# Kernel tuning notes

Measured on AMD Instinct MI355X. Metric: run time of the kernel, lower is better.

## Reference

```python
import jax, jax.numpy as jnp
import numpy as np

B, S, H, W, C = 2, 21, 256, 256, 256
Q, NEG = 256, 256
TEMP = 0.5
STRONG_T = 1.0
EPS = 1e-8


def setup_inputs():
    key = jax.random.key(0)
    k1, k2, k3 = jax.random.split(key, 3)
    rep = jax.random.normal(k1, (B, C, H, W), jnp.float32)
    label = jax.random.randint(k2, (B, 1, H, W), 0, S)
    mask = jnp.ones((B, 1, H, W), jnp.float32)
    prob = jax.random.uniform(k3, (B, S, H, W), jnp.float32)
    return {"rep": rep, "label": label, "mask": mask, "prob": prob}


def _cos(a, b, axis=-1):
    # torch.cosine_similarity: dot / (max(|a|,eps) * max(|b|,eps))
    an = jnp.maximum(jnp.linalg.norm(a, axis=axis), EPS)
    bn = jnp.maximum(jnp.linalg.norm(b, axis=axis), EPS)
    return jnp.sum(a * b, axis=axis) / (an * bn)


def _reco_loss(rep, label, mask, prob):
    Sg = prob.shape[1]
    Cf = rep.shape[1]
    lab = label.reshape(-1).astype(jnp.int32)          # [N]
    ignore = lab > Sg - 1
    lab = jnp.where(ignore, 0, lab)
    m = jnp.where(ignore, 0.0, mask.reshape(-1))
    valid = m > 0                                      # [N]
    feats = jnp.transpose(rep, (0, 2, 3, 1)).reshape(-1, Cf)   # [N,C]
    pflat = jnp.transpose(prob, (0, 2, 3, 1)).reshape(-1, Sg)  # [N,S]
    p_lab = jnp.take_along_axis(pflat, lab[:, None], axis=1)[:, 0]
    hard = valid & (p_lab < STRONG_T)

    seg_id = jnp.where(valid, lab, Sg)  # invalid pixels -> overflow bucket Sg
    counts = jax.ops.segment_sum(valid.astype(jnp.int32), seg_id, num_segments=Sg + 1)[:Sg]
    hard_counts = jax.ops.segment_sum(hard.astype(jnp.int32), seg_id, num_segments=Sg + 1)[:Sg]
    proto = jax.ops.segment_sum(feats * valid[:, None].astype(feats.dtype), seg_id,
                                num_segments=Sg + 1)[:Sg]
    proto = proto / jnp.maximum(counts, 1)[:, None].astype(feats.dtype)  # [S,C]

    # stable sort pixels by (segment, hard-first): emulates the per-segment
    # boolean-mask gathers / concatenation order of the torch code
    order = jnp.argsort(seg_id * 2 + (~hard).astype(jnp.int32))
    feats_sorted = feats[order]                                 # [N,C]
    off = jnp.concatenate([jnp.zeros((1,), counts.dtype), jnp.cumsum(counts)[:-1]])

    seg_ids = jnp.arange(Sg)
    keys = jax.random.split(jax.random.key(1), Sg)

    def body(acc, xs):
        i, ki = xs
        ka, kc, kn = jax.random.split(ki, 3)
        # anchors: num_queries random hard pixels of segment i
        hidx = off[i] + jax.random.randint(ka, (Q,), 0, jnp.maximum(hard_counts[i], 1))
        anchor = feats_sorted[hidx]                             # [Q,C]
        # negative class distribution over other segments (rolled order)
        roll = (i + 1 + jnp.arange(Sg - 1)) % Sg
        proto_logits = _cos(proto[i][None, :], proto[roll]) / TEMP  # [S-1]
        samp = jax.random.categorical(kc, proto_logits, shape=(Q, NEG))
        neg_seg = roll[samp]                                    # [Q,NEG]
        # uniform pixel within each sampled segment's block
        u = jax.random.uniform(kn, (Q, NEG))
        nidx = off[neg_seg] + jnp.floor(u * jnp.maximum(counts[neg_seg], 1)).astype(counts.dtype)
        neg_feat = feats_sorted[nidx]                           # [Q,NEG,C]
        all_feat = jnp.concatenate(
            [jnp.broadcast_to(proto[i], (Q, 1, Cf)), neg_feat], axis=1)
        all_feat = jax.lax.stop_gradient(all_feat)              # torch.no_grad block
        seg_logits = _cos(anchor[:, None, :], all_feat) / TEMP  # [Q,1+NEG]
        # cross-entropy with target 0, mean over queries
        ce = jnp.mean(jax.nn.logsumexp(seg_logits, axis=1) - seg_logits[:, 0])
        acc = acc + jnp.where(hard_counts[i] > 0, ce, 0.0)
        return acc, None

    total, _ = jax.lax.scan(body, jnp.float32(0.0), (seg_ids, keys))
    valid_seg = jnp.sum(counts > 0)
    loss = total / jnp.maximum(valid_seg, 1).astype(jnp.float32)
    return jnp.where(valid_seg > 1, loss, jnp.float32(0.0))


def reference(rep, label, mask, prob):
    loss_weight = 1.0
    return loss_weight * _reco_loss(rep, label, mask, prob)
```

## Files before the change

### kernel.cpp

```cpp
#include <hip/hip_runtime.h>
#include <stdint.h>

#define NPIX  131072
#define HW    65536
#define CCH   256
#define NSEG  21
#define NROLL 20
#define QQ    256
#define NNEG  256

typedef float f32x2 __attribute__((ext_vector_type(2)));
typedef __fp16 half2t __attribute__((ext_vector_type(2)));

__device__ __forceinline__ uint64_t rng64(uint32_t i, uint32_t q, uint32_t j) {
  uint64_t x = ((uint64_t)((i << 8) | q) << 32) | (uint64_t)(j * 0x9E3779B1u);
  x ^= 0xD1B54A32D192ED03ULL;
  x += 0x9E3779B97F4A7C15ULL;
  x = (x ^ (x >> 30)) * 0xBF58476D1CE4E5B9ULL;
  x = (x ^ (x >> 27)) * 0x94D049BB133111EBULL;
  return x ^ (x >> 31);
}

__device__ __forceinline__ float fdot2h(half2t a, half2t b, float c) {
  return __builtin_amdgcn_fdot2(a, b, c, false);
}

__device__ __forceinline__ void dec16(uint4 w, half2t* nx) {
  uint32_t dw[4] = { w.x, w.y, w.z, w.w };
#pragma unroll
  for (int d = 0; d < 4; ++d) {
    f32x2 lo = __builtin_amdgcn_cvt_pk_f32_fp8((int)dw[d], false);
    f32x2 hi = __builtin_amdgcn_cvt_pk_f32_fp8((int)dw[d], true);
    nx[d * 2 + 0] = __builtin_amdgcn_cvt_pkrtz(lo.x, lo.y);
    nx[d * 2 + 1] = __builtin_amdgcn_cvt_pkrtz(hi.x, hi.y);
  }
}

__global__ __launch_bounds__(256) void reco_zero(float4* __restrict__ zr, int n4) {
  int idx = blockIdx.x * 256 + threadIdx.x;
  if (idx < n4) zr[idx] = make_float4(0.f, 0.f, 0.f, 0.f);
}

__global__ __launch_bounds__(256) void reco_flags(
    const int* __restrict__ label, const float* __restrict__ mask,
    const float* __restrict__ prob, int* __restrict__ labh,
    int* __restrict__ counts, int* __restrict__ hardc) {
  int row = blockIdx.x;
  int b = row >> 8;
  int h = row & 255;
  int t = threadIdx.x;
  int n = row * 256 + t;

  int lab = label[n];
  bool ignore = lab > NSEG - 1;
  if (ignore) lab = 0;
  float mval = ignore ? 0.f : mask[n];
  bool valid = mval > 0.f;
  float p_lab = prob[(((size_t)b * NSEG + lab) * 256 + h) * 256 + t];
  bool hard = valid && (p_lab < 1.0f);
  labh[n] = lab | (hard ? 32 : 0) | (valid ? 64 : 0);

  __shared__ int cpart[NSEG], hpart[NSEG];
  if (t < NSEG) { cpart[t] = 0; hpart[t] = 0; }
  __syncthreads();
  if (valid) { atomicAdd(&cpart[lab], 1); if (hard) atomicAdd(&hpart[lab], 1); }
  __syncthreads();
  if (t < NSEG) {
    if (cpart[t]) atomicAdd(&counts[t], cpart[t]);
    if (hpart[t]) atomicAdd(&hardc[t], hpart[t]);
  }
}

__global__ void reco_k2t(const int* __restrict__ counts, const int* __restrict__ hardc,
                         int* __restrict__ offs, int* __restrict__ cur_h, int* __restrict__ cur_e) {
  if (threadIdx.x == 0 && blockIdx.x == 0) {
    int o = 0;
    for (int s = 0; s < NSEG; ++s) {
      offs[s] = o;
      cur_h[s] = o;
      cur_e[s] = o + hardc[s];
      o += counts[s];
    }
    offs[NSEG] = o;
  }
}

__global__ __launch_bounds__(256) void reco_k3(const int* __restrict__ labh,
                        int* __restrict__ cur_h, int* __restrict__ cur_e, int* __restrict__ list) {
  int t = threadIdx.x;
  int n = blockIdx.x * 256 + t;
  __shared__ int lcnt[2 * NSEG];
  __shared__ int lbase[2 * NSEG];
  if (t < 2 * NSEG) lcnt[t] = 0;
  __syncthreads();
  int v = labh[n];
  int lab = v & 31;
  bool hard = (v & 32) != 0;
  bool valid = (v & 64) != 0;
  int bucket = lab + (hard ? 0 : NSEG);
  int rank = 0;
  if (valid) rank = atomicAdd(&lcnt[bucket], 1);
  __syncthreads();
  if (t < 2 * NSEG) {
    int c = lcnt[t];
    lbase[t] = c ? atomicAdd((t < NSEG) ? &cur_h[t] : &cur_e[t - NSEG], c) : 0;
  }
  __syncthreads();
  if (valid) list[lbase[bucket] + rank] = n;
}

__global__ __launch_bounds__(256) void reco_k5f(const float* __restrict__ rep,
                        uint8_t* __restrict__ f8, float* __restrict__ norms) {
  int bid = blockIdx.x;
  int wtile = bid & 3;
  int row = bid >> 2;
  int b = row >> 8, h = row & 255;
  int w0 = wtile * 64;
  int t = threadIdx.x;

  __shared__ float tile[64][257];
  __shared__ float partial[4][64];
  __shared__ float inv[64];

  const float* repb = rep + (size_t)b * CCH * HW + (size_t)h * 256 + w0;
  int w4 = t & 15;
  int cbase = t >> 4;
#pragma unroll
  for (int it = 0; it < 16; ++it) {
    int c = it * 16 + cbase;
    float4 v = *(const float4*)&repb[(size_t)c * HW + w4 * 4];
    tile[w4 * 4 + 0][c] = v.x;
    tile[w4 * 4 + 1][c] = v.y;
    tile[w4 * 4 + 2][c] = v.z;
    tile[w4 * 4 + 3][c] = v.w;
  }
  __syncthreads();

  {
    int w = t & 63, qtr = t >> 6;
    float acc = 0.f;
#pragma unroll 8
    for (int cc = 0; cc < 64; ++cc) {
      float v = tile[w][qtr * 64 + cc];
      acc += v * v;
    }
    partial[qtr][w] = acc;
  }
  __syncthreads();
  if (t < 64) {
    float s = partial[0][t] + partial[1][t] + partial[2][t] + partial[3][t];
    float nm = fmaxf(sqrtf(s), 1e-8f);
    inv[t] = 1.0f / nm;
    norms[row * 256 + w0 + t] = nm;
  }
  __syncthreads();

  int pix = t & 7, chunk = t >> 3;
#pragma unroll
  for (int it = 0; it < 8; ++it) {
    int p = it * 8 + pix;
    float iv = inv[p];
    float v[8];
#pragma unroll
    for (int k = 0; k < 8; ++k) v[k] = tile[p][chunk * 8 + k] * iv;
    uint32_t lo = 0, hi = 0;
    lo = (uint32_t)__builtin_amdgcn_cvt_pk_fp8_f32(v[0], v[1], (int)lo, false);
    lo = (uint32_t)__builtin_amdgcn_cvt_pk_fp8_f32(v[2], v[3], (int)lo, true);
    hi = (uint32_t)__builtin_amdgcn_cvt_pk_fp8_f32(v[4], v[5], (int)hi, false);
    hi = (uint32_t)__builtin_amdgcn_cvt_pk_fp8_f32(v[6], v[7], (int)hi, true);
    size_t n = (size_t)(row * 256 + w0 + p);
    uint2 o; o.x = lo; o.y = hi;
    *(uint2*)&f8[n * CCH + chunk * 8] = o;
  }
}

__global__ __launch_bounds__(256) void reco_proto8(
    const uint8_t* __restrict__ f8, const float* __restrict__ norms,
    const int* __restrict__ list, const int* __restrict__ labh,
    const int* __restrict__ offs, float* __restrict__ proto) {
  int t = threadIdx.x;
  int base = blockIdx.x * 256;
  int total = offs[NSEG];

  __shared__ uint8_t rows[64][256];
  __shared__ float nrm[64];
  __shared__ int segs[256];
  __shared__ int pixs[256];
  __shared__ float red[64][17];

  {
    int pos = base + t;
    int p = (pos < total) ? (list[pos] & (NPIX - 1)) : -1;
    pixs[t] = p;
    segs[t] = (p >= 0) ? (labh[p] & 31) : -1;
  }
  __syncthreads();

  int d = t & 63;
  int qt = t >> 6;
  float a0 = 0.f, a1 = 0.f, a2 = 0.f, a3 = 0.f;
  int cseg = -2;

  for (int sub = 0; sub < 4; ++sub) {
    {
      int r = t >> 2, c = (t & 3) * 64;
      int p = pixs[sub * 64 + r];
      uint4* dst = (uint4*)&rows[r][c];
      if (p >= 0) {
        const uint4* src = (const uint4*)&f8[(size_t)p * CCH + c];
        dst[0] = src[0]; dst[1] = src[1]; dst[2] = src[2]; dst[3] = src[3];
      } else {
        uint4 z = make_uint4(0, 0, 0, 0);
        dst[0] = z; dst[1] = z; dst[2] = z; dst[3] = z;
      }
      if (t < 64) {
        int pp = pixs[sub * 64 + t];
        nrm[t] = (pp >= 0) ? norms[pp] : 0.f;
      }
    }
    __syncthreads();
    for (int pp = 0; pp < 16; ++pp) {
      int pl = qt * 16 + pp;
      int sg = segs[sub * 64 + pl];
      if (sg >= 0) {
        if (sg != cseg) {
          if (cseg >= 0) {
            atomicAdd(&proto[cseg * CCH + d * 4 + 0], a0);
            atomicAdd(&proto[cseg * CCH + d * 4 + 1], a1);
            atomicAdd(&proto[cseg * CCH + d * 4 + 2], a2);
            atomicAdd(&proto[cseg * CCH + d * 4 + 3], a3);
          }
          a0 = a1 = a2 = a3 = 0.f;
          cseg = sg;
        }
        uint32_t w = *(const uint32_t*)&rows[pl][d * 4];
        f32x2 lo = __builtin_amdgcn_cvt_pk_f32_fp8((int)w, false);
        f32x2 hi = __builtin_amdgcn_cvt_pk_f32_fp8((int)w, true);
        float nv = nrm[pl];
        a0 += lo.x * nv; a1 += lo.y * nv; a2 += hi.x * nv; a3 += hi.y * nv;
      }
    }
    __syncthreads();
  }

  int s0 = segs[0];
  int uni = __syncthreads_and((cseg < 0) || (cseg == s0));
  if (uni) {
    if (cseg >= 0) {
      red[d][qt * 4 + 0] = a0;
      red[d][qt * 4 + 1] = a1;
      red[d][qt * 4 + 2] = a2;
      red[d][qt * 4 + 3] = a3;
    }
    __syncthreads();
    if (t < 64 && s0 >= 0) {
#pragma unroll
      for (int c = 0; c < 4; ++c) {
        float v = red[t][0 + c] + red[t][4 + c] + red[t][8 + c] + red[t][12 + c];
        atomicAdd(&proto[s0 * CCH + t * 4 + c], v);
      }
    }
  } else if (cseg >= 0) {
    atomicAdd(&proto[cseg * CCH + d * 4 + 0], a0);
    atomicAdd(&proto[cseg * CCH + d * 4 + 1], a1);
    atomicAdd(&proto[cseg * CCH + d * 4 + 2], a2);
    atomicAdd(&proto[cseg * CCH + d * 4 + 3], a3);
  }
}

__global__ __launch_bounds__(256) void reco_k4(float* __restrict__ proto, float* __restrict__ protoN,
                        const int* __restrict__ counts, float* __restrict__ cdf) {
  __shared__ float pn[NSEG];
  __shared__ float spN[NSEG * CCH];
  __shared__ float lg[NSEG][NROLL];
  int t = threadIdx.x;
  for (int idx = t; idx < NSEG * CCH; idx += 256) {
    int s = idx >> 8;
    int c = counts[s]; if (c < 1) c = 1;
    proto[idx] = proto[idx] / (float)c;
  }
  __syncthreads();
  if (t < NSEG) {
    float s2 = 0.f;
    for (int c = 0; c < CCH; ++c) { float v = proto[t * CCH + c]; s2 += v * v; }
    pn[t] = fmaxf(sqrtf(s2), 1e-8f);
  }
  __syncthreads();
  for (int idx = t; idx < NSEG * CCH; idx += 256) {
    int s = idx >> 8;
    float v = proto[idx] / pn[s];
    spN[idx] = v;
    protoN[idx] = v;
  }
  __syncthreads();
  for (int idx = t; idx < NSEG * NROLL; idx += 256) {
    int i = idx / NROLL, k = idx % NROLL;
    int j = (i + 1 + k) % NSEG;
    float d = 0.f;
    for (int c = 0; c < CCH; ++c) d += spN[i * CCH + c] * spN[j * CCH + c];
    lg[i][k] = d * 2.0f;
  }
  __syncthreads();
  if (t < NSEG) {
    float mx = -1e30f;
    for (int k = 0; k < NROLL; ++k) mx = fmaxf(mx, lg[t][k]);
    float e[NROLL]; float s = 0.f;
    for (int k = 0; k < NROLL; ++k) { e[k] = __expf(lg[t][k] - mx); s += e[k]; }
    float a = 0.f;
    for (int k = 0; k < NROLL; ++k) { a += e[k] / s; cdf[t * NROLL + k] = a; }
    cdf[t * NROLL + NROLL - 1] = 2.0f;
  }
}

__global__ __launch_bounds__(256) void reco_k6h(
    const uint8_t* __restrict__ f8, const int* __restrict__ list,
    const int* __restrict__ counts, const int* __restrict__ hardc,
    const int* __restrict__ offs, const float* __restrict__ protoN,
    const float* __restrict__ cdf, float* __restrict__ seg_sum) {
  int bid = blockIdx.x;
  int i  = bid >> 5;
  int qc = bid & 31;
  int t = threadIdx.x;

  __shared__ __align__(16) char SM[65536 + 4096 + 1024];
  uint4*  negs4 = (uint4*)SM;
  half2t* anch  = (half2t*)(SM + 65536);
  float*  pNs   = (float*)(SM + 65536 + 4096);
  float*  lgts  = (float*)SM;
  __shared__ float s_cdf[NROLL];
  __shared__ int s_off[NSEG], s_cnt[NSEG], s_pidx[256], s_apix[8];
  __shared__ float s_ce[8];

  if (t < NSEG) { s_off[t] = offs[t]; s_cnt[t] = counts[t]; }
  if (t < NROLL) s_cdf[t] = cdf[i * NROLL + t];
  pNs[t] = protoN[i * CCH + t];
  if (t < 8) {
    int q = qc * 8 + t;
    uint64_t r = rng64(i, q, 511u);
    int hc = hardc[i]; if (hc < 1) hc = 1;
    uint32_t jj = (uint32_t)(r & 0xffffffffu) % (uint32_t)hc;
    int idx = offs[i] + (int)jj;
    if (idx > NPIX - 1) idx = NPIX - 1;
    s_apix[t] = list[idx] & (NPIX - 1);
  }
  __syncthreads();

  {
    uint64_t r = rng64(i, 0u, (uint32_t)(t + 1));
    float u1 = (float)(r >> 40) * (1.0f / 16777216.0f);
    float u2 = (float)((r >> 16) & 0xFFFFFFu) * (1.0f / 16777216.0f);
    int k = 0;
#pragma unroll
    for (int kk = 0; kk < NROLL - 1; ++kk) k += (u1 >= s_cdf[kk]);
    int seg = i + 1 + k; if (seg >= NSEG) seg -= NSEG;
    int cnt = s_cnt[seg]; int cm = cnt < 1 ? 1 : cnt;
    int pidx = (int)(u2 * (float)cm);
    if (pidx > cm - 1) pidx = cm - 1;
    int li = s_off[seg] + pidx;
    if (li > NPIX - 1) li = NPIX - 1;
    s_pidx[t] = list[li] & (NPIX - 1);
  }
  if (t < 128) {
    int g = t >> 4, x = t & 15;
    uint4 w = *(const uint4*)&f8[(size_t)s_apix[g] * CCH + x * 16];
    half2t dx[8]; dec16(w, dx);
#pragma unroll
    for (int k = 0; k < 8; ++k) anch[g * 128 + x * 8 + k] = dx[k];
  }
  __syncthreads();

  int g2 = t >> 4, x2 = t & 15;
  uint4 rst[16];
#pragma unroll
  for (int k = 0; k < 16; ++k) {
    int r = k * 16 + g2;
    rst[k] = *(const uint4*)&f8[(size_t)s_pidx[r] * CCH + x2 * 16];
  }
#pragma unroll
  for (int k = 0; k < 16; ++k) {
    int r = k * 16 + g2;
    negs4[r * 16 + (x2 ^ (r & 15))] = rst[k];
  }
  __syncthreads();

  float acc[8];
#pragma unroll
  for (int q = 0; q < 8; ++q) acc[q] = 0.f;
  for (int c16 = 0; c16 < 16; ++c16) {
    uint4 w = negs4[t * 16 + (c16 ^ (t & 15))];
    half2t nx[8]; dec16(w, nx);
    const half2t* ar = anch + c16 * 8;
#pragma unroll
    for (int q = 0; q < 8; ++q) {
      const half2t* a = ar + q * 128;
      float s = acc[q];
#pragma unroll
      for (int k = 0; k < 8; ++k) s = fdot2h(a[k], nx[k], s);
      acc[q] = s;
    }
  }
  float ps = 0.f;
  if (t < 128) {
    int g = t >> 4, x = t & 15;
#pragma unroll
    for (int k = 0; k < 8; ++k) {
      half2t a = anch[g * 128 + x * 8 + k];
      ps += (float)a.x * pNs[x * 16 + 2 * k] + (float)a.y * pNs[x * 16 + 2 * k + 1];
    }
#pragma unroll
    for (int o = 1; o <= 8; o <<= 1) ps += __shfl_xor(ps, o);
  }
  __syncthreads();

#pragma unroll
  for (int q = 0; q < 8; ++q) lgts[q * 264 + 1 + t] = acc[q] * 2.0f;
  if (t < 128 && (t & 15) == 0) lgts[(t >> 4) * 264 + 0] = ps * 2.0f;
  __syncthreads();

  int wave = t >> 6, lane = t & 63;
  for (int q = wave; q < 8; q += 4) {
    const float* L = lgts + q * 264;
    float v0 = L[lane], v1 = L[lane + 64], v2 = L[lane + 128], v3 = L[lane + 192];
    float v4 = (lane == 0) ? L[256] : -1e30f;
    float m = fmaxf(fmaxf(fmaxf(v0, v1), fmaxf(v2, v3)), v4);
#pragma unroll
    for (int o = 32; o >= 1; o >>= 1) m = fmaxf(m, __shfl_xor(m, o));
    float e = __expf(v0 - m) + __expf(v1 - m) + __expf(v2 - m) + __expf(v3 - m)
            + ((lane == 0) ? __expf(v4 - m) : 0.f);
#pragma unroll
    for (int o = 32; o >= 1; o >>= 1) e += __shfl_xor(e, o);
    if (lane == 0) s_ce[q] = m + logf(e) - L[0];
  }
  __syncthreads();
  if (t == 0) {
    float s = 0.f;
#pragma unroll
    for (int q = 0; q < 8; ++q) s += s_ce[q];
    atomicAdd(&seg_sum[i], s);
  }
}

__global__ void reco_k7(const float* __restrict__ seg_sum, const int* __restrict__ counts,
                        const int* __restrict__ hardc, float* __restrict__ out) {
  if (threadIdx.x == 0 && blockIdx.x == 0) {
    float tot = 0.f; int vs = 0;
    for (int s = 0; s < NSEG; ++s) {
      vs += (counts[s] > 0);
      if (hardc[s] > 0) tot += seg_sum[s];
    }
    float loss = (tot * (1.0f / 256.0f)) / (float)(vs > 0 ? vs : 1);
    out[0] = (vs > 1) ? loss : 0.f;
  }
}

extern "C" void kernel_launch(void* const* d_in, const int* in_sizes, int n_in,
                              void* d_out, int out_size, void* d_ws, size_t ws_size,
                              hipStream_t stream) {
  const float* rep   = (const float*)d_in[0];
  const int*   label = (const int*)d_in[1];
  const float* mask  = (const float*)d_in[2];
  const float* prob  = (const float*)d_in[3];

  char* ws = (char*)d_ws;
  uint8_t* f8 = (uint8_t*)ws;
  size_t o = 67108864;
  float* norms  = (float*)(ws + o); o += 524288;
  int*   list   = (int*)(ws + o);   o += 524288;
  int*   labh   = (int*)(ws + o);   o += 524288;
  float* proto  = (float*)(ws + o); o += 21504;
  int*   counts = (int*)(ws + o);   o += 128;
  int*   hardc  = (int*)(ws + o);   o += 128;
  float* segsum = (float*)(ws + o); o += 128;
  int*   offs   = (int*)(ws + o);   o += 128;
  int*   cur_h  = (int*)(ws + o);   o += 128;
  int*   cur_e  = (int*)(ws + o);   o += 128;
  float* protoN = (float*)(ws + o); o += 21504;
  float* cdf    = (float*)(ws + o); o += 2048;

  reco_zero<<<6, 256, 0, stream>>>((float4*)proto, 1368);

  reco_flags<<<512, 256, 0, stream>>>(label, mask, prob, labh, counts, hardc);
  reco_k2t<<<1, 1, 0, stream>>>(counts, hardc, offs, cur_h, cur_e);
  reco_k3<<<512, 256, 0, stream>>>(labh, cur_h, cur_e, list);
  reco_k5f<<<2048, 256, 0, stream>>>(rep, f8, norms);
  reco_proto8<<<512, 256, 0, stream>>>(f8, norms, list, labh, offs, proto);
  reco_k4<<<1, 256, 0, stream>>>(proto, protoN, counts, cdf);
  reco_k6h<<<NSEG * 32, 256, 0, stream>>>(f8, list, counts, hardc, offs, protoN, cdf, segsum);
  reco_k7<<<1, 1, 0, stream>>>(segsum, counts, hardc, (float*)d_out);
}
```

Measured before the change: 126.7 us.

## Pre-gather negatives per segment, fuse zeroing and final reduce, drop global atomics

```diff
diff --git a/kernel.cpp b/kernel.cpp
--- a/kernel.cpp
+++ b/kernel.cpp
@@ -36,20 +36,20 @@
   }
 }
 
-__global__ __launch_bounds__(256) void reco_zero(float4* __restrict__ zr, int n4) {
-  int idx = blockIdx.x * 256 + threadIdx.x;
-  if (idx < n4) zr[idx] = make_float4(0.f, 0.f, 0.f, 0.f);
-}
-
 __global__ __launch_bounds__(256) void reco_flags(
     const int* __restrict__ label, const float* __restrict__ mask,
     const float* __restrict__ prob, int* __restrict__ labh,
-    int* __restrict__ counts, int* __restrict__ hardc) {
+    int* __restrict__ bc, float4* __restrict__ zr) {
   int row = blockIdx.x;
   int b = row >> 8;
   int h = row & 255;
   int t = threadIdx.x;
   int n = row * 256 + t;
+
+  if (row < 6) {
+    int idx = row * 256 + t;
+    if (idx < 1360) zr[idx] = make_float4(0.f, 0.f, 0.f, 0.f);
+  }
 
   int lab = label[n];
   bool ignore = lab > NSEG - 1;
@@ -66,20 +66,32 @@
   if (valid) { atomicAdd(&cpart[lab], 1); if (hard) atomicAdd(&hpart[lab], 1); }
   __syncthreads();
   if (t < NSEG) {
-    if (cpart[t]) atomicAdd(&counts[t], cpart[t]);
-    if (hpart[t]) atomicAdd(&hardc[t], hpart[t]);
-  }
-}
-
-__global__ void reco_k2t(const int* __restrict__ counts, const int* __restrict__ hardc,
-                         int* __restrict__ offs, int* __restrict__ cur_h, int* __restrict__ cur_e) {
-  if (threadIdx.x == 0 && blockIdx.x == 0) {
+    bc[row * 48 + t] = cpart[t];
+    bc[row * 48 + 24 + t] = hpart[t];
+  }
+}
+
+__global__ void reco_k2t(const int* __restrict__ bc, int* __restrict__ counts,
+                         int* __restrict__ hardc, int* __restrict__ offs,
+                         int* __restrict__ cur_h, int* __restrict__ cur_e) {
+  int t = threadIdx.x;
+  __shared__ int cnt[NSEG], hrd[NSEG];
+  if (t < 42) {
+    int c = (t < 21) ? t : t + 3;
+    int s = 0;
+#pragma unroll 8
+    for (int r = 0; r < 512; ++r) s += bc[r * 48 + c];
+    if (t < 21) { cnt[t] = s; counts[t] = s; }
+    else        { hrd[t - 21] = s; hardc[t - 21] = s; }
+  }
+  __syncthreads();
+  if (t == 0) {
     int o = 0;
     for (int s = 0; s < NSEG; ++s) {
       offs[s] = o;
       cur_h[s] = o;
-      cur_e[s] = o + hardc[s];
-      o += counts[s];
+      cur_e[s] = o + hrd[s];
+      o += cnt[s];
     }
     offs[NSEG] = o;
   }
@@ -312,27 +324,56 @@
   }
 }
 
+__global__ __launch_bounds__(256) void reco_knegs(
+    const uint8_t* __restrict__ f8, const int* __restrict__ list,
+    const int* __restrict__ counts, const int* __restrict__ offs,
+    const float* __restrict__ cdf, uint8_t* __restrict__ negbuf) {
+  int i = blockIdx.x;
+  int t = threadIdx.x;
+  __shared__ float s_cdf[NROLL];
+  __shared__ int s_off[NSEG], s_cnt[NSEG];
+  if (t < NSEG) { s_off[t] = offs[t]; s_cnt[t] = counts[t]; }
+  if (t < NROLL) s_cdf[t] = cdf[i * NROLL + t];
+  __syncthreads();
+
+  uint64_t r = rng64(i, 0u, (uint32_t)(t + 1));
+  float u1 = (float)(r >> 40) * (1.0f / 16777216.0f);
+  float u2 = (float)((r >> 16) & 0xFFFFFFu) * (1.0f / 16777216.0f);
+  int k = 0;
+#pragma unroll
+  for (int kk = 0; kk < NROLL - 1; ++kk) k += (u1 >= s_cdf[kk]);
+  int seg = i + 1 + k; if (seg >= NSEG) seg -= NSEG;
+  int cnt = s_cnt[seg]; int cm = cnt < 1 ? 1 : cnt;
+  int pidx = (int)(u2 * (float)cm);
+  if (pidx > cm - 1) pidx = cm - 1;
+  int li = s_off[seg] + pidx;
+  if (li > NPIX - 1) li = NPIX - 1;
+  int p = list[li] & (NPIX - 1);
+
+  const uint4* src = (const uint4*)&f8[(size_t)p * CCH];
+  uint4* dst = (uint4*)&negbuf[((size_t)i * 256 + t) * CCH];
+#pragma unroll
+  for (int c = 0; c < 16; ++c) dst[c] = src[c];
+}
+
 __global__ __launch_bounds__(256) void reco_k6h(
-    const uint8_t* __restrict__ f8, const int* __restrict__ list,
-    const int* __restrict__ counts, const int* __restrict__ hardc,
-    const int* __restrict__ offs, const float* __restrict__ protoN,
-    const float* __restrict__ cdf, float* __restrict__ seg_sum) {
+    const uint8_t* __restrict__ f8, const uint8_t* __restrict__ negbuf,
+    const int* __restrict__ list, const int* __restrict__ counts,
+    const int* __restrict__ hardc, const int* __restrict__ offs,
+    const float* __restrict__ protoN, float* __restrict__ seg_sum,
+    int* __restrict__ ticket, float* __restrict__ out) {
   int bid = blockIdx.x;
   int i  = bid >> 5;
   int qc = bid & 31;
   int t = threadIdx.x;
 
-  __shared__ __align__(16) char SM[65536 + 4096 + 1024];
-  uint4*  negs4 = (uint4*)SM;
-  half2t* anch  = (half2t*)(SM + 65536);
-  float*  pNs   = (float*)(SM + 65536 + 4096);
-  float*  lgts  = (float*)SM;
-  __shared__ float s_cdf[NROLL];
-  __shared__ int s_off[NSEG], s_cnt[NSEG], s_pidx[256], s_apix[8];
+  __shared__ half2t anch[8 * 128];
+  __shared__ float pNs[256];
+  __shared__ float lgts[8][264];
+  __shared__ int s_apix[8];
   __shared__ float s_ce[8];
-
-  if (t < NSEG) { s_off[t] = offs[t]; s_cnt[t] = counts[t]; }
-  if (t < NROLL) s_cdf[t] = cdf[i * NROLL + t];
+  __shared__ int s_last;
+
   pNs[t] = protoN[i * CCH + t];
   if (t < 8) {
     int q = qc * 8 + t;
@@ -344,22 +385,6 @@
     s_apix[t] = list[idx] & (NPIX - 1);
   }
   __syncthreads();
-
-  {
-    uint64_t r = rng64(i, 0u, (uint32_t)(t + 1));
-    float u1 = (float)(r >> 40) * (1.0f / 16777216.0f);
-    float u2 = (float)((r >> 16) & 0xFFFFFFu) * (1.0f / 16777216.0f);
-    int k = 0;
-#pragma unroll
-    for (int kk = 0; kk < NROLL - 1; ++kk) k += (u1 >= s_cdf[kk]);
-    int seg = i + 1 + k; if (seg >= NSEG) seg -= NSEG;
-    int cnt = s_cnt[seg]; int cm = cnt < 1 ? 1 : cnt;
-    int pidx = (int)(u2 * (float)cm);
-    if (pidx > cm - 1) pidx = cm - 1;
-    int li = s_off[seg] + pidx;
-    if (li > NPIX - 1) li = NPIX - 1;
-    s_pidx[t] = list[li] & (NPIX - 1);
-  }
   if (t < 128) {
     int g = t >> 4, x = t & 15;
     uint4 w = *(const uint4*)&f8[(size_t)s_apix[g] * CCH + x * 16];
@@ -369,34 +394,26 @@
   }
   __syncthreads();
 
-  int g2 = t >> 4, x2 = t & 15;
-  uint4 rst[16];
-#pragma unroll
-  for (int k = 0; k < 16; ++k) {
-    int r = k * 16 + g2;
-    rst[k] = *(const uint4*)&f8[(size_t)s_pidx[r] * CCH + x2 * 16];
-  }
-#pragma unroll
-  for (int k = 0; k < 16; ++k) {
-    int r = k * 16 + g2;
-    negs4[r * 16 + (x2 ^ (r & 15))] = rst[k];
-  }
-  __syncthreads();
-
+  const uint4* rowp = (const uint4*)&negbuf[((size_t)i * 256 + t) * CCH];
   float acc[8];
 #pragma unroll
   for (int q = 0; q < 8; ++q) acc[q] = 0.f;
-  for (int c16 = 0; c16 < 16; ++c16) {
-    uint4 w = negs4[t * 16 + (c16 ^ (t & 15))];
-    half2t nx[8]; dec16(w, nx);
-    const half2t* ar = anch + c16 * 8;
-#pragma unroll
-    for (int q = 0; q < 8; ++q) {
-      const half2t* a = ar + q * 128;
-      float s = acc[q];
-#pragma unroll
-      for (int k = 0; k < 8; ++k) s = fdot2h(a[k], nx[k], s);
-      acc[q] = s;
+  for (int k0 = 0; k0 < 16; k0 += 4) {
+    uint4 w4[4];
+#pragma unroll
+    for (int u = 0; u < 4; ++u) w4[u] = rowp[k0 + u];
+#pragma unroll
+    for (int u = 0; u < 4; ++u) {
+      half2t nx[8]; dec16(w4[u], nx);
+      const half2t* ar = anch + (k0 + u) * 8;
+#pragma unroll
+      for (int q = 0; q < 8; ++q) {
+        const half2t* a = ar + q * 128;
+        float s = acc[q];
+#pragma unroll
+        for (int k = 0; k < 8; ++k) s = fdot2h(a[k], nx[k], s);
+        acc[q] = s;
+      }
     }
   }
   float ps = 0.f;
@@ -410,16 +427,15 @@
 #pragma unroll
     for (int o = 1; o <= 8; o <<= 1) ps += __shfl_xor(ps, o);
   }
-  __syncthreads();
-
-#pragma unroll
-  for (int q = 0; q < 8; ++q) lgts[q * 264 + 1 + t] = acc[q] * 2.0f;
-  if (t < 128 && (t & 15) == 0) lgts[(t >> 4) * 264 + 0] = ps * 2.0f;
+
+#pragma unroll
+  for (int q = 0; q < 8; ++q) lgts[q][1 + t] = acc[q] * 2.0f;
+  if (t < 128 && (t & 15) == 0) lgts[t >> 4][0] = ps * 2.0f;
   __syncthreads();
 
   int wave = t >> 6, lane = t & 63;
   for (int q = wave; q < 8; q += 4) {
-    const float* L = lgts + q * 264;
+    const float* L = lgts[q];
     float v0 = L[lane], v1 = L[lane + 64], v2 = L[lane + 128], v3 = L[lane + 192];
     float v4 = (lane == 0) ? L[256] : -1e30f;
     float m = fmaxf(fmaxf(fmaxf(v0, v1), fmaxf(v2, v3)), v4);
@@ -437,16 +453,18 @@
 #pragma unroll
     for (int q = 0; q < 8; ++q) s += s_ce[q];
     atomicAdd(&seg_sum[i], s);
-  }
-}
-
-__global__ void reco_k7(const float* __restrict__ seg_sum, const int* __restrict__ counts,
-                        const int* __restrict__ hardc, float* __restrict__ out) {
-  if (threadIdx.x == 0 && blockIdx.x == 0) {
+    __threadfence();
+    int done = atomicAdd(ticket, 1);
+    s_last = (done == NSEG * 32 - 1);
+  }
+  __syncthreads();
+  if (s_last && t == 0) {
+    __threadfence();
     float tot = 0.f; int vs = 0;
     for (int s = 0; s < NSEG; ++s) {
       vs += (counts[s] > 0);
-      if (hardc[s] > 0) tot += seg_sum[s];
+      float v = atomicAdd(&seg_sum[s], 0.f);
+      if (hardc[s] > 0) tot += v;
     }
     float loss = (tot * (1.0f / 256.0f)) / (float)(vs > 0 ? vs : 1);
     out[0] = (vs > 1) ? loss : 0.f;
@@ -468,23 +486,25 @@
   int*   list   = (int*)(ws + o);   o += 524288;
   int*   labh   = (int*)(ws + o);   o += 524288;
   float* proto  = (float*)(ws + o); o += 21504;
+  float* segsum = (float*)(ws + o); o += 128;
+  int*   ticket = (int*)(ws + o);   o += 128;
   int*   counts = (int*)(ws + o);   o += 128;
   int*   hardc  = (int*)(ws + o);   o += 128;
-  float* segsum = (float*)(ws + o); o += 128;
   int*   offs   = (int*)(ws + o);   o += 128;
   int*   cur_h  = (int*)(ws + o);   o += 128;
   int*   cur_e  = (int*)(ws + o);   o += 128;
   float* protoN = (float*)(ws + o); o += 21504;
   float* cdf    = (float*)(ws + o); o += 2048;
-
-  reco_zero<<<6, 256, 0, stream>>>((float4*)proto, 1368);
-
-  reco_flags<<<512, 256, 0, stream>>>(label, mask, prob, labh, counts, hardc);
-  reco_k2t<<<1, 1, 0, stream>>>(counts, hardc, offs, cur_h, cur_e);
+  uint8_t* negbuf = (uint8_t*)(ws + o); o += 1376256;
+  int*   bc     = (int*)(ws + o);   o += 98304;
+
+  reco_flags<<<512, 256, 0, stream>>>(label, mask, prob, labh, bc, (float4*)proto);
+  reco_k2t<<<1, 64, 0, stream>>>(bc, counts, hardc, offs, cur_h, cur_e);
   reco_k3<<<512, 256, 0, stream>>>(labh, cur_h, cur_e, list);
   reco_k5f<<<2048, 256, 0, stream>>>(rep, f8, norms);
   reco_proto8<<<512, 256, 0, stream>>>(f8, norms, list, labh, offs, proto);
   reco_k4<<<1, 256, 0, stream>>>(proto, protoN, counts, cdf);
-  reco_k6h<<<NSEG * 32, 256, 0, stream>>>(f8, list, counts, hardc, offs, protoN, cdf, segsum);
-  reco_k7<<<1, 1, 0, stream>>>(segsum, counts, hardc, (float*)d_out);
-}
+  reco_knegs<<<NSEG, 256, 0, stream>>>(f8, list, counts, offs, cdf, negbuf);
+  reco_k6h<<<NSEG * 32, 256, 0, stream>>>(f8, negbuf, list, counts, hardc, offs,
+                                          protoN, segsum, ticket, (float*)d_out);
+}
```

After: 135.8 us. 7.2% more time.
